# Performance work log

Measured on AMD Instinct MI355X. Metric: run time of the kernel, lower is better.

Reference implementation:

```python
import jax, jax.numpy as jnp
import numpy as np

B, S, D, H = 2, 2048, 1024, 16
HD = D // H  # 64

def setup_inputs() -> dict:
    key = jax.random.key(0)
    k1, k2, k3 = jax.random.split(key, 3)
    hidden_states = jax.random.normal(k1, (B, S, D), dtype=jnp.float32)
    w_attn = jax.random.normal(k2, (D, 3 * D), dtype=jnp.float32) * 0.02
    w_proj = jax.random.normal(k3, (D, D), dtype=jnp.float32) * 0.02
    return {"hidden_states": hidden_states, "w_attn": w_attn, "w_proj": w_proj}

def reference(hidden_states, w_attn, w_proj):
    b, s, d = hidden_states.shape
    # c_attn: Conv1D (bias is a scalar zero in the source)
    qkv = jnp.einsum('bsd,de->bse', hidden_states, w_attn)  # [B,S,3D]
    q, k, v = jnp.split(qkv, 3, axis=-1)
    def split_heads(t):
        return t.reshape(b, s, H, HD).transpose(0, 2, 1, 3)  # [B,H,S,HD]
    q, k, v = split_heads(q), split_heads(k), split_heads(v)
    # eager attention; scale_attn_weights=True -> divide by sqrt(head_dim)
    scores = jnp.einsum('bhqd,bhkd->bhqk', q, k) / jnp.sqrt(jnp.float32(HD))
    # NOTE: source registers bias buffer as all-ones (True), so the causal
    # torch.where is a no-op -- faithfully no masking is applied.
    probs = jax.nn.softmax(scores, axis=-1)
    attn = jnp.einsum('bhqk,bhkd->bhqd', probs, v)  # [B,H,S,HD]
    attn = attn.transpose(0, 2, 1, 3).reshape(b, s, d)  # merge heads
    out = jnp.einsum('bsd,de->bse', attn, w_proj)  # c_proj (zero bias)
    return out
```

## Files before the change

kernel.cpp:

```cpp
#include <hip/hip_runtime.h>
#include <hip/hip_bf16.h>

typedef __attribute__((ext_vector_type(8))) short bf16x8;
typedef __attribute__((ext_vector_type(4))) short short4v;
typedef __attribute__((ext_vector_type(4))) float f32x4;
typedef __attribute__((ext_vector_type(16))) float f32x16;
typedef __attribute__((ext_vector_type(4))) float float4v;

__device__ __forceinline__ short f2bf(float f) {
    union { float f; unsigned u; } v; v.f = f;
    unsigned r = v.u + 0x7fffu + ((v.u >> 16) & 1u);
    return (short)(r >> 16);
}
__device__ __forceinline__ float bf2f(short s) {
    union { unsigned u; float f; } v;
    v.u = ((unsigned)(unsigned short)s) << 16;
    return v.f;
}

__device__ __forceinline__ void gload16(const short* g, short* lds) {
    __builtin_amdgcn_global_load_lds(
        (const __attribute__((address_space(1))) unsigned*)g,
        (__attribute__((address_space(3))) unsigned*)lds, 16, 0, 0);
}

__device__ __forceinline__ void tconv_tile(const float* __restrict__ in,
                                           short* __restrict__ out,
                                           int Kdim, int Ndim, int n0, int k0) {
    __shared__ int Ls[64][65];
    const int t = threadIdx.x;
    const int kl = t >> 4, n4 = (t & 15) * 4;
#pragma unroll
    for (int it = 0; it < 4; ++it) {
        int k = kl + it * 16;
        float4v v = *reinterpret_cast<const float4v*>(&in[(size_t)(k0 + k) * Ndim + n0 + n4]);
#pragma unroll
        for (int c = 0; c < 4; ++c) Ls[k][n4 + c] = (int)(unsigned short)f2bf(v[c]);
    }
    __syncthreads();
    const int nl0 = t >> 4, kq = (t & 15) * 4;
#pragma unroll
    for (int it = 0; it < 4; ++it) {
        int nl = nl0 + it * 16;
        short4v s;
#pragma unroll
        for (int j = 0; j < 4; ++j) s[j] = (short)Ls[kq + j][nl];
        *reinterpret_cast<short4v*>(&out[(size_t)(n0 + nl) * Kdim + k0 + kq]) = s;
    }
}

__global__ __launch_bounds__(256) void prep1(const float* __restrict__ hidden,
                                             short* __restrict__ Ah,
                                             const float* __restrict__ w_attn,
                                             short* __restrict__ Wta) {
    const int bx = blockIdx.x;
    if (bx < 2048) {
        int i = (bx * 256 + threadIdx.x) * 8;
        float4v a0 = *reinterpret_cast<const float4v*>(&hidden[i]);
        float4v a1 = *reinterpret_cast<const float4v*>(&hidden[i + 4]);
        bf16x8 s;
        s[0] = f2bf(a0[0]); s[1] = f2bf(a0[1]); s[2] = f2bf(a0[2]); s[3] = f2bf(a0[3]);
        s[4] = f2bf(a1[0]); s[5] = f2bf(a1[1]); s[6] = f2bf(a1[2]); s[7] = f2bf(a1[3]);
        *reinterpret_cast<bf16x8*>(&Ah[i]) = s;
    } else {
        int idx = bx - 2048;
        int n0 = (idx % 48) * 64, k0 = (idx / 48) * 64;
        tconv_tile(w_attn, Wta, 1024, 3072, n0, k0);
    }
}

__global__ __launch_bounds__(256) void qkv_gemm(const short* __restrict__ Ah,
                                                const short* __restrict__ Wt,
                                                short* __restrict__ Qw,
                                                short* __restrict__ Kw,
                                                short* __restrict__ Vt) {
    __shared__ short As[128 * 64];
    __shared__ short Bs[128 * 64];
    const int tid = threadIdx.x;
    const int l = tid & 63, w = tid >> 6;
    const int g = l >> 4, lr = l & 15;
    const int r8 = l >> 3, sl = l & 7;
    const int xs = (sl ^ r8) * 8;
    const int wm = (w >> 1) * 64, wn = (w & 1) * 64;
    const int bid = blockIdx.x;
    const int xcd = bid & 7, idx = bid >> 3;
    const int nt = (xcd & 1) * 12 + idx % 12;
    const int mt = (xcd >> 1) * 8 + idx / 12;
    const int m0 = mt * 128;
    const int n0 = nt * 128;
    const bool isV = (n0 >= 2048);
    f32x4 acc[4][4] = {};
    for (int k0 = 0; k0 < 1024; k0 += 64) {
        const short* Ag = Ah + m0 * 1024 + k0;
        const short* Bg = Wt + n0 * 1024 + k0;
#pragma unroll
        for (int i = 0; i < 4; ++i) {
            int seg = w * 4 + i;
            gload16(Ag + (seg * 8 + r8) * 1024 + xs, &As[seg * 512]);
            gload16(Bg + (seg * 8 + r8) * 1024 + xs, &Bs[seg * 512]);
        }
        __syncthreads();
#pragma unroll
        for (int kk = 0; kk < 2; ++kk) {
            bf16x8 af[4], bfr[4];
#pragma unroll
            for (int mi = 0; mi < 4; ++mi) {
                int row = wm + mi * 16 + lr;
                af[mi] = *reinterpret_cast<const bf16x8*>(&As[row * 64 + (((4 * kk + g) ^ (lr & 7)) * 8)]);
            }
#pragma unroll
            for (int ni = 0; ni < 4; ++ni) {
                int col = wn + ni * 16 + lr;
                bfr[ni] = *reinterpret_cast<const bf16x8*>(&Bs[col * 64 + (((4 * kk + g) ^ (lr & 7)) * 8)]);
            }
            if (isV) {
#pragma unroll
                for (int mi = 0; mi < 4; ++mi)
#pragma unroll
                    for (int ni = 0; ni < 4; ++ni)
                        acc[mi][ni] = __builtin_amdgcn_mfma_f32_16x16x32_bf16(af[mi], bfr[ni], acc[mi][ni], 0, 0, 0);
            } else {
#pragma unroll
                for (int mi = 0; mi < 4; ++mi)
#pragma unroll
                    for (int ni = 0; ni < 4; ++ni)
                        acc[mi][ni] = __builtin_amdgcn_mfma_f32_16x16x32_bf16(bfr[ni], af[mi], acc[mi][ni], 0, 0, 0);
            }
        }
        __syncthreads();
    }
    if (isV) {
#pragma unroll
        for (int mi = 0; mi < 4; ++mi) {
            int m = m0 + wm + mi * 16 + g * 4;
            int bb = m >> 11, s0 = m & 2047;
#pragma unroll
            for (int ni = 0; ni < 4; ++ni) {
                int n = n0 + wn + ni * 16 + lr;
                int hh = (n >> 6) & 15, d = n & 63;
                short4v pv;
#pragma unroll
                for (int r = 0; r < 4; ++r) pv[r] = f2bf(acc[mi][ni][r]);
                *reinterpret_cast<short4v*>(&Vt[(((bb * 16 + hh) * 64) + d) * 2048 + s0]) = pv;
            }
        }
    } else {
        const bool isQ = (n0 < 1024);
        const float sc = isQ ? 0.18033688011112042f : 1.0f;
        short* dst = isQ ? Qw : Kw;
#pragma unroll
        for (int mi = 0; mi < 4; ++mi) {
            int m = m0 + wm + mi * 16 + lr;
            int bb = m >> 11, s0 = m & 2047;
#pragma unroll
            for (int ni = 0; ni < 4; ++ni) {
                int n = n0 + wn + ni * 16 + g * 4;
                int hh = (n >> 6) & 15, d = n & 63;
                float a0 = acc[mi][ni][0] * sc, a1 = acc[mi][ni][1] * sc;
                float a2 = acc[mi][ni][2] * sc, a3 = acc[mi][ni][3] * sc;
                int w0, w1;
                asm("v_cvt_pk_bf16_f32 %0, %1, %2" : "=v"(w0) : "v"(a0), "v"(a1));
                asm("v_cvt_pk_bf16_f32 %0, %1, %2" : "=v"(w1) : "v"(a2), "v"(a3));
                union { int wd[2]; short4v s; } u;
                u.wd[0] = w0; u.wd[1] = w1;
                *reinterpret_cast<short4v*>(&dst[((bb * 16 + hh) * 2048 + s0) * 64 + d]) = u.s;
            }
        }
    }
}

__global__ __launch_bounds__(256, 4) void attn6s(const short* __restrict__ Qw,
                                                 const short* __restrict__ Kw,
                                                 const short* __restrict__ Vt,
                                                 short* __restrict__ N0,
                                                 short* __restrict__ N1,
                                                 float* __restrict__ Tot) {
    __shared__ short Ks[2][64 * 64];
    __shared__ short Vs[2][64 * 64];
    const int tid = threadIdx.x;
    const int w = tid >> 6, l = tid & 63;
    const int q = l & 31, hi = l >> 5;
    const int r8 = l >> 3, sl = l & 7;
    const int xs = (sl ^ r8) * 8;
    const int bid = blockIdx.x;
    const int work = (bid & 7) * 128 + (bid >> 3);
    const int head = work >> 5;
    const int qblk = (work & 31) >> 1;
    const int ks = work & 1;
    const int b = head >> 4, h = head & 15;
    const int q0 = qblk * 128 + w * 32;
    const short* Qb = Qw + ((b * 16 + h) * 2048 + q0) * 64;
    const short* Kb = Kw + ((b * 16 + h) * 2048 + ks * 1024) * 64;
    const short* Vb = Vt + ((b * 16 + h) * 64) * 2048 + ks * 1024;

    bf16x8 qb[4];
#pragma unroll
    for (int c = 0; c < 4; ++c)
        qb[c] = *reinterpret_cast<const bf16x8*>(&Qb[q * 64 + c * 16 + hi * 8]);

    int koff[2][4], voff[2][2][2];
#pragma unroll
    for (int sub = 0; sub < 2; ++sub)
#pragma unroll
        for (int c = 0; c < 4; ++c)
            koff[sub][c] = (sub * 32 + q) * 64 + (((2 * c + hi) ^ (q & 7)) * 8);
#pragma unroll
    for (int sub = 0; sub < 2; ++sub)
#pragma unroll
        for (int c2 = 0; c2 < 2; ++c2)
#pragma unroll
            for (int dt = 0; dt < 2; ++dt)
                voff[sub][c2][dt] = (dt * 32 + q) * 64 + (((4 * sub + 2 * c2 + hi) ^ (q & 7)) * 8);

    f32x16 o0 = {}, o1 = {};
    float psum = 0.f;

#define STAGE_KV(buf, j0)                                                        \
    {                                                                            \
        _Pragma("unroll")                                                        \
        for (int i = 0; i < 2; ++i) {                                            \
            int seg = w * 2 + i;                                                 \
            gload16(Kb + ((j0) + seg * 8 + r8) * 64 + xs, &Ks[buf][seg * 512]);  \
            gload16(Vb + (seg * 8 + r8) * 2048 + (j0) + xs, &Vs[buf][seg * 512]);\
        }                                                                        \
    }

    STAGE_KV(0, 0);
    __syncthreads();
    int cur = 0;

    for (int jt = 0; jt < 16; ++jt) {
        if (jt < 15) STAGE_KV(cur ^ 1, (jt + 1) * 64);

#pragma unroll
        for (int sub = 0; sub < 2; ++sub) {
            f32x16 st = {};
            __builtin_amdgcn_s_setprio(1);
#pragma unroll
            for (int c = 0; c < 4; ++c) {
                bf16x8 ka = *reinterpret_cast<const bf16x8*>(&Ks[cur][koff[sub][c]]);
                st = __builtin_amdgcn_mfma_f32_32x32x16_bf16(ka, qb[c], st, 0, 0, 0);
            }
            __builtin_amdgcn_s_setprio(0);
            float p[16];
#pragma unroll
            for (int r = 0; r < 16; ++r) p[r] = __builtin_amdgcn_exp2f(st[r]);
            float s01 = (p[0] + p[1]) + (p[2] + p[3]);
            float s23 = (p[4] + p[5]) + (p[6] + p[7]);
            float s45 = (p[8] + p[9]) + (p[10] + p[11]);
            float s67 = (p[12] + p[13]) + (p[14] + p[15]);
            psum += (s01 + s23) + (s45 + s67);
            int pk[4][2];
#pragma unroll
            for (int bq = 0; bq < 4; ++bq) {
                int w0, w1;
                asm("v_cvt_pk_bf16_f32 %0, %1, %2" : "=v"(w0) : "v"(p[4 * bq]), "v"(p[4 * bq + 1]));
                asm("v_cvt_pk_bf16_f32 %0, %1, %2" : "=v"(w1) : "v"(p[4 * bq + 2]), "v"(p[4 * bq + 3]));
                pk[bq][0] = w0; pk[bq][1] = w1;
            }
#pragma unroll
            for (int c2 = 0; c2 < 2; ++c2) {
                int w0 = pk[2 * c2][0], w2 = pk[2 * c2 + 1][0];
                int w1 = pk[2 * c2][1], w3 = pk[2 * c2 + 1][1];
                asm("v_permlane32_swap_b32 %0, %1" : "+v"(w0), "+v"(w2));
                asm("v_permlane32_swap_b32 %0, %1" : "+v"(w1), "+v"(w3));
                union { int wd[4]; bf16x8 v; } pb;
                pb.wd[0] = w0; pb.wd[1] = w1; pb.wd[2] = w2; pb.wd[3] = w3;
                __builtin_amdgcn_s_setprio(1);
#pragma unroll
                for (int dt = 0; dt < 2; ++dt) {
                    bf16x8 va = *reinterpret_cast<const bf16x8*>(&Vs[cur][voff[sub][c2][dt]]);
                    if (dt == 0) o0 = __builtin_amdgcn_mfma_f32_32x32x16_bf16(va, pb.v, o0, 0, 0, 0);
                    else         o1 = __builtin_amdgcn_mfma_f32_32x32x16_bf16(va, pb.v, o1, 0, 0, 0);
                }
                __builtin_amdgcn_s_setprio(0);
            }
        }
        __syncthreads();
        cur ^= 1;
    }
#undef STAGE_KV

    int pa = __float_as_int(psum), pb2 = pa;
    asm("v_permlane32_swap_b32 %0, %1" : "+v"(pa), "+v"(pb2));
    float tot = __int_as_float(pa) + __int_as_float(pb2);
    float inv = 1.f / tot;

    short* Nd = ks ? N1 : N0;
    short* Orow = &Nd[(b * 2048 + q0 + q) * 1024 + h * 64];
#pragma unroll
    for (int r = 0; r < 4; ++r) {
        short4v ov0, ov1;
#pragma unroll
        for (int j = 0; j < 4; ++j) {
            ov0[j] = f2bf(o0[4 * r + j] * inv);
            ov1[j] = f2bf(o1[4 * r + j] * inv);
        }
        *reinterpret_cast<short4v*>(&Orow[8 * r + 4 * hi]) = ov0;
        *reinterpret_cast<short4v*>(&Orow[32 + 8 * r + 4 * hi]) = ov1;
    }
    if (hi == 0)
        Tot[ks * 65536 + (b * 16 + h) * 2048 + q0 + q] = tot;
}

__global__ __launch_bounds__(256) void post(short* __restrict__ N0,
                                            const short* __restrict__ N1,
                                            const float* __restrict__ Tot,
                                            const float* __restrict__ w_proj,
                                            short* __restrict__ Wtp) {
    const int bx = blockIdx.x;
    if (bx < 2048) {
        int i = (bx * 256 + threadIdx.x) * 8;
        int bs = i >> 10;
        int b = bs >> 11, s = bs & 2047;
        int h = (i >> 6) & 15;
        int qi = (b * 16 + h) * 2048 + s;
        float t0 = Tot[qi], t1 = Tot[65536 + qi];
        float inv = 1.f / (t0 + t1);
        float w0 = t0 * inv, w1 = t1 * inv;
        bf16x8 a = *reinterpret_cast<const bf16x8*>(&N0[i]);
        bf16x8 c = *reinterpret_cast<const bf16x8*>(&N1[i]);
        bf16x8 r;
#pragma unroll
        for (int j = 0; j < 8; ++j) r[j] = f2bf(bf2f(a[j]) * w0 + bf2f(c[j]) * w1);
        *reinterpret_cast<bf16x8*>(&N0[i]) = r;
    } else {
        int idx = bx - 2048;
        int n0 = (idx % 16) * 64, k0 = (idx / 16) * 64;
        tconv_tile(w_proj, Wtp, 1024, 1024, n0, k0);
    }
}

__global__ __launch_bounds__(256) void proj_gemm(const short* __restrict__ Ag,
                                                 const short* __restrict__ Wtp,
                                                 float* __restrict__ Out) {
    __shared__ short As[128 * 64];
    __shared__ short Bs[128 * 64];
    const int tid = threadIdx.x;
    const int l = tid & 63, w = tid >> 6;
    const int g = l >> 4, lr = l & 15;
    const int r8 = l >> 3, sl = l & 7;
    const int xs = (sl ^ r8) * 8;
    const int wm = (w >> 1) * 64, wn = (w & 1) * 64;
    const int bid = blockIdx.x;
    const int xcd = bid & 7, idx = bid >> 3;
    const int nt = (xcd & 1) * 4 + (idx & 3);
    const int mt = (xcd >> 1) * 8 + (idx >> 2);
    const int m0 = mt * 128;
    const int n0 = nt * 128;
    f32x4 acc[4][4] = {};
    for (int k0 = 0; k0 < 1024; k0 += 64) {
        const short* Ab = Ag + m0 * 1024 + k0;
        const short* Bg = Wtp + n0 * 1024 + k0;
#pragma unroll
        for (int i = 0; i < 4; ++i) {
            int seg = w * 4 + i;
            gload16(Ab + (seg * 8 + r8) * 1024 + xs, &As[seg * 512]);
            gload16(Bg + (seg * 8 + r8) * 1024 + xs, &Bs[seg * 512]);
        }
        __syncthreads();
#pragma unroll
        for (int kk = 0; kk < 2; ++kk) {
            bf16x8 af[4], bfr[4];
#pragma unroll
            for (int mi = 0; mi < 4; ++mi) {
                int row = wm + mi * 16 + lr;
                af[mi] = *reinterpret_cast<const bf16x8*>(&As[row * 64 + (((4 * kk + g) ^ (lr & 7)) * 8)]);
            }
#pragma unroll
            for (int ni = 0; ni < 4; ++ni) {
                int col = wn + ni * 16 + lr;
                bfr[ni] = *reinterpret_cast<const bf16x8*>(&Bs[col * 64 + (((4 * kk + g) ^ (lr & 7)) * 8)]);
            }
#pragma unroll
            for (int mi = 0; mi < 4; ++mi)
#pragma unroll
                for (int ni = 0; ni < 4; ++ni)
                    acc[mi][ni] = __builtin_amdgcn_mfma_f32_16x16x32_bf16(af[mi], bfr[ni], acc[mi][ni], 0, 0, 0);
        }
        __syncthreads();
    }
#pragma unroll
    for (int mi = 0; mi < 4; ++mi) {
#pragma unroll
        for (int ni = 0; ni < 4; ++ni) {
            int n = n0 + wn + ni * 16 + lr;
#pragma unroll
            for (int r = 0; r < 4; ++r) {
                int mm = m0 + wm + mi * 16 + g * 4 + r;
                Out[mm * 1024 + n] = acc[mi][ni][r];
            }
        }
    }
}

extern "C" void kernel_launch(void* const* d_in, const int* in_sizes, int n_in,
                              void* d_out, int out_size, void* d_ws, size_t ws_size,
                              hipStream_t stream) {
    const float* hidden = (const float*)d_in[0];
    const float* w_attn = (const float*)d_in[1];
    const float* w_proj = (const float*)d_in[2];
    float* out = (float*)d_out;

    short* AhN0 = (short*)d_ws;
    short* Qw = AhN0 + 4194304;
    short* Kw = Qw + 4194304;
    short* Vt = Kw + 4194304;
    short* Wta = (short*)d_out;
    float* Tot = (float*)((char*)d_out + 7u * 1024 * 1024);
    short* N1 = (short*)((char*)d_out + 8u * 1024 * 1024);

    prep1<<<dim3(2816), 256, 0, stream>>>(hidden, AhN0, w_attn, Wta);
    qkv_gemm<<<dim3(768), 256, 0, stream>>>(AhN0, Wta, Qw, Kw, Vt);
    attn6s<<<dim3(1024), 256, 0, stream>>>(Qw, Kw, Vt, AhN0, N1, Tot);
    post<<<dim3(2304), 256, 0, stream>>>(AhN0, N1, Tot, w_proj, Qw);
    proj_gemm<<<dim3(256), 256, 0, stream>>>(AhN0, Qw, out);
}
```

Measured before the change: 126.1 us.

## Process two 32-row query tiles per wave in attention to reuse K/V fragments

```diff
diff --git a/kernel.cpp b/kernel.cpp
--- a/kernel.cpp
+++ b/kernel.cpp
@@ -169,12 +169,12 @@
     }
 }
 
-__global__ __launch_bounds__(256, 4) void attn6s(const short* __restrict__ Qw,
-                                                 const short* __restrict__ Kw,
-                                                 const short* __restrict__ Vt,
-                                                 short* __restrict__ N0,
-                                                 short* __restrict__ N1,
-                                                 float* __restrict__ Tot) {
+__global__ __launch_bounds__(128, 2) void attn8(const short* __restrict__ Qw,
+                                                const short* __restrict__ Kw,
+                                                const short* __restrict__ Vt,
+                                                short* __restrict__ N0,
+                                                short* __restrict__ N1,
+                                                float* __restrict__ Tot) {
     __shared__ short Ks[2][64 * 64];
     __shared__ short Vs[2][64 * 64];
     const int tid = threadIdx.x;
@@ -188,15 +188,17 @@
     const int qblk = (work & 31) >> 1;
     const int ks = work & 1;
     const int b = head >> 4, h = head & 15;
-    const int q0 = qblk * 128 + w * 32;
-    const short* Qb = Qw + ((b * 16 + h) * 2048 + q0) * 64;
+    const int q0w = qblk * 128 + w * 64;
+    const short* Qb = Qw + ((b * 16 + h) * 2048 + q0w) * 64;
     const short* Kb = Kw + ((b * 16 + h) * 2048 + ks * 1024) * 64;
     const short* Vb = Vt + ((b * 16 + h) * 64) * 2048 + ks * 1024;
 
-    bf16x8 qb[4];
-#pragma unroll
-    for (int c = 0; c < 4; ++c)
-        qb[c] = *reinterpret_cast<const bf16x8*>(&Qb[q * 64 + c * 16 + hi * 8]);
+    bf16x8 qb0[4], qb1[4];
+#pragma unroll
+    for (int c = 0; c < 4; ++c) {
+        qb0[c] = *reinterpret_cast<const bf16x8*>(&Qb[q * 64 + c * 16 + hi * 8]);
+        qb1[c] = *reinterpret_cast<const bf16x8*>(&Qb[(32 + q) * 64 + c * 16 + hi * 8]);
+    }
 
     int koff[2][4], voff[2][2][2];
 #pragma unroll
@@ -212,14 +214,15 @@
             for (int dt = 0; dt < 2; ++dt)
                 voff[sub][c2][dt] = (dt * 32 + q) * 64 + (((4 * sub + 2 * c2 + hi) ^ (q & 7)) * 8);
 
-    f32x16 o0 = {}, o1 = {};
-    float psum = 0.f;
+    f32x16 oA0 = {}, oA1 = {};
+    f32x16 oB0 = {}, oB1 = {};
+    float psumA = 0.f, psumB = 0.f;
 
 #define STAGE_KV(buf, j0)                                                        \
     {                                                                            \
         _Pragma("unroll")                                                        \
-        for (int i = 0; i < 2; ++i) {                                            \
-            int seg = w * 2 + i;                                                 \
+        for (int i = 0; i < 4; ++i) {                                            \
+            int seg = w * 4 + i;                                                 \
             gload16(Kb + ((j0) + seg * 8 + r8) * 64 + xs, &Ks[buf][seg * 512]);  \
             gload16(Vb + (seg * 8 + r8) * 2048 + (j0) + xs, &Vs[buf][seg * 512]);\
         }                                                                        \
@@ -234,44 +237,61 @@
 
 #pragma unroll
         for (int sub = 0; sub < 2; ++sub) {
-            f32x16 st = {};
+            bf16x8 ka[4];
+#pragma unroll
+            for (int c = 0; c < 4; ++c)
+                ka[c] = *reinterpret_cast<const bf16x8*>(&Ks[cur][koff[sub][c]]);
+            f32x16 stA = {}, stB = {};
             __builtin_amdgcn_s_setprio(1);
 #pragma unroll
             for (int c = 0; c < 4; ++c) {
-                bf16x8 ka = *reinterpret_cast<const bf16x8*>(&Ks[cur][koff[sub][c]]);
-                st = __builtin_amdgcn_mfma_f32_32x32x16_bf16(ka, qb[c], st, 0, 0, 0);
+                stA = __builtin_amdgcn_mfma_f32_32x32x16_bf16(ka[c], qb0[c], stA, 0, 0, 0);
+                stB = __builtin_amdgcn_mfma_f32_32x32x16_bf16(ka[c], qb1[c], stB, 0, 0, 0);
             }
             __builtin_amdgcn_s_setprio(0);
-            float p[16];
-#pragma unroll
-            for (int r = 0; r < 16; ++r) p[r] = __builtin_amdgcn_exp2f(st[r]);
-            float s01 = (p[0] + p[1]) + (p[2] + p[3]);
-            float s23 = (p[4] + p[5]) + (p[6] + p[7]);
-            float s45 = (p[8] + p[9]) + (p[10] + p[11]);
-            float s67 = (p[12] + p[13]) + (p[14] + p[15]);
-            psum += (s01 + s23) + (s45 + s67);
-            int pk[4][2];
+            float pA[16], pB[16];
+#pragma unroll
+            for (int r = 0; r < 16; ++r) pA[r] = __builtin_amdgcn_exp2f(stA[r]);
+#pragma unroll
+            for (int r = 0; r < 16; ++r) pB[r] = __builtin_amdgcn_exp2f(stB[r]);
+            psumA += ((pA[0] + pA[1]) + (pA[2] + pA[3])) + ((pA[4] + pA[5]) + (pA[6] + pA[7]))
+                   + ((pA[8] + pA[9]) + (pA[10] + pA[11])) + ((pA[12] + pA[13]) + (pA[14] + pA[15]));
+            psumB += ((pB[0] + pB[1]) + (pB[2] + pB[3])) + ((pB[4] + pB[5]) + (pB[6] + pB[7]))
+                   + ((pB[8] + pB[9]) + (pB[10] + pB[11])) + ((pB[12] + pB[13]) + (pB[14] + pB[15]));
+            int pkA[4][2], pkB[4][2];
 #pragma unroll
             for (int bq = 0; bq < 4; ++bq) {
-                int w0, w1;
-                asm("v_cvt_pk_bf16_f32 %0, %1, %2" : "=v"(w0) : "v"(p[4 * bq]), "v"(p[4 * bq + 1]));
-                asm("v_cvt_pk_bf16_f32 %0, %1, %2" : "=v"(w1) : "v"(p[4 * bq + 2]), "v"(p[4 * bq + 3]));
-                pk[bq][0] = w0; pk[bq][1] = w1;
+                int w0, w1, w2, w3;
+                asm("v_cvt_pk_bf16_f32 %0, %1, %2" : "=v"(w0) : "v"(pA[4 * bq]), "v"(pA[4 * bq + 1]));
+                asm("v_cvt_pk_bf16_f32 %0, %1, %2" : "=v"(w1) : "v"(pA[4 * bq + 2]), "v"(pA[4 * bq + 3]));
+                asm("v_cvt_pk_bf16_f32 %0, %1, %2" : "=v"(w2) : "v"(pB[4 * bq]), "v"(pB[4 * bq + 1]));
+                asm("v_cvt_pk_bf16_f32 %0, %1, %2" : "=v"(w3) : "v"(pB[4 * bq + 2]), "v"(pB[4 * bq + 3]));
+                pkA[bq][0] = w0; pkA[bq][1] = w1;
+                pkB[bq][0] = w2; pkB[bq][1] = w3;
             }
 #pragma unroll
             for (int c2 = 0; c2 < 2; ++c2) {
-                int w0 = pk[2 * c2][0], w2 = pk[2 * c2 + 1][0];
-                int w1 = pk[2 * c2][1], w3 = pk[2 * c2 + 1][1];
-                asm("v_permlane32_swap_b32 %0, %1" : "+v"(w0), "+v"(w2));
-                asm("v_permlane32_swap_b32 %0, %1" : "+v"(w1), "+v"(w3));
-                union { int wd[4]; bf16x8 v; } pb;
-                pb.wd[0] = w0; pb.wd[1] = w1; pb.wd[2] = w2; pb.wd[3] = w3;
+                int a0 = pkA[2 * c2][0], a2 = pkA[2 * c2 + 1][0];
+                int a1 = pkA[2 * c2][1], a3 = pkA[2 * c2 + 1][1];
+                asm("v_permlane32_swap_b32 %0, %1" : "+v"(a0), "+v"(a2));
+                asm("v_permlane32_swap_b32 %0, %1" : "+v"(a1), "+v"(a3));
+                int b0 = pkB[2 * c2][0], b2 = pkB[2 * c2 + 1][0];
+                int b1 = pkB[2 * c2][1], b3 = pkB[2 * c2 + 1][1];
+                asm("v_permlane32_swap_b32 %0, %1" : "+v"(b0), "+v"(b2));
+                asm("v_permlane32_swap_b32 %0, %1" : "+v"(b1), "+v"(b3));
+                union { int wd[4]; bf16x8 v; } pa, pbv;
+                pa.wd[0] = a0; pa.wd[1] = a1; pa.wd[2] = a2; pa.wd[3] = a3;
+                pbv.wd[0] = b0; pbv.wd[1] = b1; pbv.wd[2] = b2; pbv.wd[3] = b3;
                 __builtin_amdgcn_s_setprio(1);
-#pragma unroll
-                for (int dt = 0; dt < 2; ++dt) {
-                    bf16x8 va = *reinterpret_cast<const bf16x8*>(&Vs[cur][voff[sub][c2][dt]]);
-                    if (dt == 0) o0 = __builtin_amdgcn_mfma_f32_32x32x16_bf16(va, pb.v, o0, 0, 0, 0);
-                    else         o1 = __builtin_amdgcn_mfma_f32_32x32x16_bf16(va, pb.v, o1, 0, 0, 0);
+                {
+                    bf16x8 va = *reinterpret_cast<const bf16x8*>(&Vs[cur][voff[sub][c2][0]]);
+                    oA0 = __builtin_amdgcn_mfma_f32_32x32x16_bf16(va, pa.v, oA0, 0, 0, 0);
+                    oB0 = __builtin_amdgcn_mfma_f32_32x32x16_bf16(va, pbv.v, oB0, 0, 0, 0);
+                }
+                {
+                    bf16x8 va = *reinterpret_cast<const bf16x8*>(&Vs[cur][voff[sub][c2][1]]);
+                    oA1 = __builtin_amdgcn_mfma_f32_32x32x16_bf16(va, pa.v, oA1, 0, 0, 0);
+                    oB1 = __builtin_amdgcn_mfma_f32_32x32x16_bf16(va, pbv.v, oB1, 0, 0, 0);
                 }
                 __builtin_amdgcn_s_setprio(0);
             }
@@ -281,26 +301,36 @@
     }
 #undef STAGE_KV
 
-    int pa = __float_as_int(psum), pb2 = pa;
-    asm("v_permlane32_swap_b32 %0, %1" : "+v"(pa), "+v"(pb2));
-    float tot = __int_as_float(pa) + __int_as_float(pb2);
-    float inv = 1.f / tot;
+    int pa0 = __float_as_int(psumA), pa1 = pa0;
+    asm("v_permlane32_swap_b32 %0, %1" : "+v"(pa0), "+v"(pa1));
+    float totA = __int_as_float(pa0) + __int_as_float(pa1);
+    int pb0 = __float_as_int(psumB), pb1 = pb0;
+    asm("v_permlane32_swap_b32 %0, %1" : "+v"(pb0), "+v"(pb1));
+    float totB = __int_as_float(pb0) + __int_as_float(pb1);
+    float invA = 1.f / totA, invB = 1.f / totB;
 
     short* Nd = ks ? N1 : N0;
-    short* Orow = &Nd[(b * 2048 + q0 + q) * 1024 + h * 64];
+    short* OrowA = &Nd[(b * 2048 + q0w + q) * 1024 + h * 64];
+    short* OrowB = &Nd[(b * 2048 + q0w + 32 + q) * 1024 + h * 64];
 #pragma unroll
     for (int r = 0; r < 4; ++r) {
-        short4v ov0, ov1;
+        short4v v0, v1, v2, v3;
 #pragma unroll
         for (int j = 0; j < 4; ++j) {
-            ov0[j] = f2bf(o0[4 * r + j] * inv);
-            ov1[j] = f2bf(o1[4 * r + j] * inv);
-        }
-        *reinterpret_cast<short4v*>(&Orow[8 * r + 4 * hi]) = ov0;
-        *reinterpret_cast<short4v*>(&Orow[32 + 8 * r + 4 * hi]) = ov1;
-    }
-    if (hi == 0)
-        Tot[ks * 65536 + (b * 16 + h) * 2048 + q0 + q] = tot;
+            v0[j] = f2bf(oA0[4 * r + j] * invA);
+            v1[j] = f2bf(oA1[4 * r + j] * invA);
+            v2[j] = f2bf(oB0[4 * r + j] * invB);
+            v3[j] = f2bf(oB1[4 * r + j] * invB);
+        }
+        *reinterpret_cast<short4v*>(&OrowA[8 * r + 4 * hi]) = v0;
+        *reinterpret_cast<short4v*>(&OrowA[32 + 8 * r + 4 * hi]) = v1;
+        *reinterpret_cast<short4v*>(&OrowB[8 * r + 4 * hi]) = v2;
+        *reinterpret_cast<short4v*>(&OrowB[32 + 8 * r + 4 * hi]) = v3;
+    }
+    if (hi == 0) {
+        Tot[ks * 65536 + (b * 16 + h) * 2048 + q0w + q] = totA;
+        Tot[ks * 65536 + (b * 16 + h) * 2048 + q0w + 32 + q] = totB;
+    }
 }
 
 __global__ __launch_bounds__(256) void post(short* __restrict__ N0,
@@ -412,7 +442,7 @@
 
     prep1<<<dim3(2816), 256, 0, stream>>>(hidden, AhN0, w_attn, Wta);
     qkv_gemm<<<dim3(768), 256, 0, stream>>>(AhN0, Wta, Qw, Kw, Vt);
-    attn6s<<<dim3(1024), 256, 0, stream>>>(Qw, Kw, Vt, AhN0, N1, Tot);
+    attn8<<<dim3(1024), 128, 0, stream>>>(Qw, Kw, Vt, AhN0, N1, Tot);
     post<<<dim3(2304), 256, 0, stream>>>(AhN0, N1, Tot, w_proj, Qw);
     proj_gemm<<<dim3(256), 256, 0, stream>>>(AhN0, Qw, out);
 }
```

After: 123.8 us. No clear change (-1.8%).

## Double-buffer LDS tiles in QKV and projection GEMMs to overlap loads with MFMA

Applied to the files above, without the earlier changes.

```diff
diff --git a/kernel.cpp b/kernel.cpp
--- a/kernel.cpp
+++ b/kernel.cpp
@@ -74,8 +74,8 @@
                                                 short* __restrict__ Qw,
                                                 short* __restrict__ Kw,
                                                 short* __restrict__ Vt) {
-    __shared__ short As[128 * 64];
-    __shared__ short Bs[128 * 64];
+    __shared__ short As[2][128 * 64];
+    __shared__ short Bs[2][128 * 64];
     const int tid = threadIdx.x;
     const int l = tid & 63, w = tid >> 6;
     const int g = l >> 4, lr = l & 15;
@@ -90,28 +90,36 @@
     const int n0 = nt * 128;
     const bool isV = (n0 >= 2048);
     f32x4 acc[4][4] = {};
-    for (int k0 = 0; k0 < 1024; k0 += 64) {
-        const short* Ag = Ah + m0 * 1024 + k0;
-        const short* Bg = Wt + n0 * 1024 + k0;
-#pragma unroll
-        for (int i = 0; i < 4; ++i) {
-            int seg = w * 4 + i;
-            gload16(Ag + (seg * 8 + r8) * 1024 + xs, &As[seg * 512]);
-            gload16(Bg + (seg * 8 + r8) * 1024 + xs, &Bs[seg * 512]);
-        }
-        __syncthreads();
+
+#define STAGE_AB(buf, k0)                                                     \
+    {                                                                         \
+        const short* Ag = Ah + m0 * 1024 + (k0);                              \
+        const short* Bg = Wt + n0 * 1024 + (k0);                              \
+        _Pragma("unroll")                                                     \
+        for (int i = 0; i < 4; ++i) {                                         \
+            int seg = w * 4 + i;                                              \
+            gload16(Ag + (seg * 8 + r8) * 1024 + xs, &As[buf][seg * 512]);    \
+            gload16(Bg + (seg * 8 + r8) * 1024 + xs, &Bs[buf][seg * 512]);    \
+        }                                                                     \
+    }
+
+    STAGE_AB(0, 0);
+    __syncthreads();
+    int cur = 0;
+    for (int kt = 0; kt < 16; ++kt) {
+        if (kt < 15) STAGE_AB(cur ^ 1, (kt + 1) * 64);
 #pragma unroll
         for (int kk = 0; kk < 2; ++kk) {
             bf16x8 af[4], bfr[4];
 #pragma unroll
             for (int mi = 0; mi < 4; ++mi) {
                 int row = wm + mi * 16 + lr;
-                af[mi] = *reinterpret_cast<const bf16x8*>(&As[row * 64 + (((4 * kk + g) ^ (lr & 7)) * 8)]);
+                af[mi] = *reinterpret_cast<const bf16x8*>(&As[cur][row * 64 + (((4 * kk + g) ^ (lr & 7)) * 8)]);
             }
 #pragma unroll
             for (int ni = 0; ni < 4; ++ni) {
                 int col = wn + ni * 16 + lr;
-                bfr[ni] = *reinterpret_cast<const bf16x8*>(&Bs[col * 64 + (((4 * kk + g) ^ (lr & 7)) * 8)]);
+                bfr[ni] = *reinterpret_cast<const bf16x8*>(&Bs[cur][col * 64 + (((4 * kk + g) ^ (lr & 7)) * 8)]);
             }
             if (isV) {
 #pragma unroll
@@ -128,7 +136,10 @@
             }
         }
         __syncthreads();
-    }
+        cur ^= 1;
+    }
+#undef STAGE_AB
+
     if (isV) {
 #pragma unroll
         for (int mi = 0; mi < 4; ++mi) {
@@ -334,8 +345,8 @@
 __global__ __launch_bounds__(256) void proj_gemm(const short* __restrict__ Ag,
                                                  const short* __restrict__ Wtp,
                                                  float* __restrict__ Out) {
-    __shared__ short As[128 * 64];
-    __shared__ short Bs[128 * 64];
+    __shared__ short As[2][128 * 64];
+    __shared__ short Bs[2][128 * 64];
     const int tid = threadIdx.x;
     const int l = tid & 63, w = tid >> 6;
     const int g = l >> 4, lr = l & 15;
@@ -349,28 +360,36 @@
     const int m0 = mt * 128;
     const int n0 = nt * 128;
     f32x4 acc[4][4] = {};
-    for (int k0 = 0; k0 < 1024; k0 += 64) {
-        const short* Ab = Ag + m0 * 1024 + k0;
-        const short* Bg = Wtp + n0 * 1024 + k0;
-#pragma unroll
-        for (int i = 0; i < 4; ++i) {
-            int seg = w * 4 + i;
-            gload16(Ab + (seg * 8 + r8) * 1024 + xs, &As[seg * 512]);
-            gload16(Bg + (seg * 8 + r8) * 1024 + xs, &Bs[seg * 512]);
-        }
-        __syncthreads();
+
+#define STAGE_AB(buf, k0)                                                     \
+    {                                                                         \
+        const short* Ab = Ag + m0 * 1024 + (k0);                              \
+        const short* Bg = Wtp + n0 * 1024 + (k0);                             \
+        _Pragma("unroll")                                                     \
+        for (int i = 0; i < 4; ++i) {                                         \
+            int seg = w * 4 + i;                                              \
+            gload16(Ab + (seg * 8 + r8) * 1024 + xs, &As[buf][seg * 512]);    \
+            gload16(Bg + (seg * 8 + r8) * 1024 + xs, &Bs[buf][seg * 512]);    \
+        }                                                                     \
+    }
+
+    STAGE_AB(0, 0);
+    __syncthreads();
+    int cur = 0;
+    for (int kt = 0; kt < 16; ++kt) {
+        if (kt < 15) STAGE_AB(cur ^ 1, (kt + 1) * 64);
 #pragma unroll
         for (int kk = 0; kk < 2; ++kk) {
             bf16x8 af[4], bfr[4];
 #pragma unroll
             for (int mi = 0; mi < 4; ++mi) {
                 int row = wm + mi * 16 + lr;
-                af[mi] = *reinterpret_cast<const bf16x8*>(&As[row * 64 + (((4 * kk + g) ^ (lr & 7)) * 8)]);
+                af[mi] = *reinterpret_cast<const bf16x8*>(&As[cur][row * 64 + (((4 * kk + g) ^ (lr & 7)) * 8)]);
             }
 #pragma unroll
             for (int ni = 0; ni < 4; ++ni) {
                 int col = wn + ni * 16 + lr;
-                bfr[ni] = *reinterpret_cast<const bf16x8*>(&Bs[col * 64 + (((4 * kk + g) ^ (lr & 7)) * 8)]);
+                bfr[ni] = *reinterpret_cast<const bf16x8*>(&Bs[cur][col * 64 + (((4 * kk + g) ^ (lr & 7)) * 8)]);
             }
 #pragma unroll
             for (int mi = 0; mi < 4; ++mi)
@@ -379,7 +398,10 @@
                     acc[mi][ni] = __builtin_amdgcn_mfma_f32_16x16x32_bf16(af[mi], bfr[ni], acc[mi][ni], 0, 0, 0);
         }
         __syncthreads();
-    }
+        cur ^= 1;
+    }
+#undef STAGE_AB
+
 #pragma unroll
     for (int mi = 0; mi < 4; ++mi) {
 #pragma unroll
```

Measured after the change: 125.6 us. Within noise of the previous version (-0.4%).
